# Kernel optimization log

Hardware: AMD Instinct MI355X
Metric: run time of the kernel (lower is better)

## Reference

```python
import jax, jax.numpy as jnp
import numpy as np

N_NODES = 50000


def gcn_conv(x, W, b, src, dst, norm, n):
    # PyG GCNConv: h = x W; out[dst] += norm * h[src]; out += b
    h = x @ W  # [N, out_dim]
    msg = h[src] * norm[:, None]  # [E+N, out_dim]
    out = jax.ops.segment_sum(msg, dst, num_segments=n)
    return out + b


def _norm_coeffs(src, dst, n):
    # symmetric normalization D^-1/2 A_hat D^-1/2 (self-loops already appended)
    deg = jax.ops.segment_sum(jnp.ones(src.shape[0], jnp.float32), dst, num_segments=n)
    dis = jnp.where(deg > 0, jax.lax.rsqrt(jnp.maximum(deg, 1.0)), 0.0)
    return dis[src] * dis[dst]


def setup_inputs() -> dict:
    key = jax.random.key(0)
    ks = jax.random.split(key, 8)
    n, e = N_NODES, 640000
    d_in, d_h, d_out = 128, 128, 64
    x = jax.random.normal(ks[0], (n, d_in), jnp.float32)
    edge_index = jax.random.randint(ks[1], (2, e), 0, n, jnp.int64)
    def glorot(k, shape):
        lim = np.sqrt(6.0 / (shape[0] + shape[1]))
        return jax.random.uniform(k, shape, jnp.float32, -lim, lim)
    return {
        "x": x,
        "edge_index": edge_index,
        "W1": glorot(ks[2], (d_in, d_h)), "b1": jnp.zeros((d_h,), jnp.float32),
        "W2": glorot(ks[3], (d_h, d_h)), "b2": jnp.zeros((d_h,), jnp.float32),
        "W3": glorot(ks[4], (d_h, d_out)), "b3": jnp.zeros((d_out,), jnp.float32),
    }


def reference(x, edge_index, W1, b1, W2, b2, W3, b3):
    n = x.shape[0]
    loop = jnp.arange(n, dtype=edge_index.dtype)
    src = jnp.concatenate([edge_index[0], loop])
    dst = jnp.concatenate([edge_index[1], loop])
    norm = _norm_coeffs(src, dst, n)
    h = jax.nn.relu(gcn_conv(x, W1, b1, src, dst, norm, n))
    h = jax.nn.relu(gcn_conv(h, W2, b2, src, dst, norm, n))
    return gcn_conv(h, W3, b3, src, dst, norm, n)
```

## Files before the change

kernel.cpp:

```cpp
#include <hip/hip_runtime.h>
#include <hip/hip_fp16.h>

typedef _Float16 f16x8 __attribute__((ext_vector_type(8)));
typedef float f32x4 __attribute__((ext_vector_type(4)));


__global__ void k_init(int* __restrict__ deg32, int nDeg,
                       unsigned int* __restrict__ ellw, int nEllw,
                       unsigned int pat) {
    int i = blockIdx.x * blockDim.x + threadIdx.x;
    if (i < nDeg) deg32[i] = 0;
    if (i < nEllw) ellw[i] = pat;
}

__global__ __launch_bounds__(256) void k_ellfill(const int* __restrict__ src,
                                                 const int* __restrict__ dst,
                                                 int* __restrict__ deg32,
                                                 unsigned short* __restrict__ ell, int E) {
    int e = blockIdx.x * blockDim.x + threadIdx.x;
    if (e >= E) return;
    int d = dst[e];
    int c = atomicAdd(&deg32[d << 4], 1);
    if (c < 64) ell[(size_t)d * 64 + c] = (unsigned short)src[e];
}

template <int BN, int NT, bool IN_F32>
__global__ __launch_bounds__(256) void k_gemm_mfma(const void* __restrict__ Xv,
                                                   const float* __restrict__ W,
                                                   const int* __restrict__ deg32,
                                                   _Float16* __restrict__ G, int N) {
    if (blockIdx.x == 0 && threadIdx.x < BN / 2)
        ((int*)(G + (size_t)N * BN))[threadIdx.x] = 0;

    const int lane = threadIdx.x & 63;
    const int wv = threadIdx.x >> 6;
    const int lo = lane & 15;
    const int kg = lane >> 4;
    const int colbase = wv * NT * 16;

    f16x8 b[4][NT];
#pragma unroll
    for (int t = 0; t < 4; ++t)
#pragma unroll
        for (int u = 0; u < NT; ++u)
#pragma unroll
            for (int j = 0; j < 8; ++j)
                b[t][u][j] = (_Float16)W[(size_t)(t * 32 + kg * 8 + j) * BN +
                                         colbase + u * 16 + lo];

    const float* Xf = (const float*)Xv;
    const _Float16* Xh = (const _Float16*)Xv;

    const int nslabs = N >> 4;
    for (int slab = blockIdx.x; slab < nslabs; slab += gridDim.x) {
        const int arow = slab * 16 + lo;
        f32x4 acc[NT];
#pragma unroll
        for (int u = 0; u < NT; ++u) acc[u] = (f32x4)0.0f;

#pragma unroll
        for (int t = 0; t < 4; ++t) {
            f16x8 a;
            if constexpr (IN_F32) {
                const float4* xp = (const float4*)&Xf[(size_t)arow * 128 + t * 32 + kg * 8];
                float4 u0 = xp[0], u1 = xp[1];
                a[0] = (_Float16)u0.x; a[1] = (_Float16)u0.y;
                a[2] = (_Float16)u0.z; a[3] = (_Float16)u0.w;
                a[4] = (_Float16)u1.x; a[5] = (_Float16)u1.y;
                a[6] = (_Float16)u1.z; a[7] = (_Float16)u1.w;
            } else {
                a = *(const f16x8*)&Xh[(size_t)arow * 128 + t * 32 + kg * 8];
            }
#pragma unroll
            for (int u = 0; u < NT; ++u)
                acc[u] = __builtin_amdgcn_mfma_f32_16x16x32_f16(a, b[t][u], acc[u], 0, 0, 0);
        }

        float ds[4];
#pragma unroll
        for (int r = 0; r < 4; ++r)
            ds[r] = rsqrtf((float)(deg32[(slab * 16 + kg * 4 + r) << 4] + 1));

#pragma unroll
        for (int u = 0; u < NT; ++u) {
            int col = colbase + u * 16 + lo;
#pragma unroll
            for (int r = 0; r < 4; ++r) {
                int row = slab * 16 + kg * 4 + r;
                G[(size_t)row * BN + col] = (_Float16)(acc[u][r] * ds[r]);
            }
        }
    }
}

__global__ __launch_bounds__(256) void k_aggr128(const int* __restrict__ deg32,
                                                 const unsigned short* __restrict__ ell,
                                                 const __half* __restrict__ gin,
                                                 const float* __restrict__ bias,
                                                 __half* __restrict__ out, int N) {
    int wid = blockIdx.x * 4 + (threadIdx.x >> 6);
    int lane = threadIdx.x & 63;
    if (wid >= N) return;
    int d = deg32[wid << 4];
    int dc = min(d, 64);
    int dp = (dc + 15) & ~15;

    const __half2* gp = (const __half2*)gin;
    float2 self = __half22float2(gp[(size_t)wid * 64 + lane]);

    const uint4* rowq = (const uint4*)&ell[(size_t)wid * 64];
    __half2 s0 = __float2half2_rn(0.f), s1 = s0, s2 = s0, s3 = s0;

    for (int j = 0; j < dp; j += 16) {
        uint4 r0 = rowq[j >> 3];
        uint4 r1 = rowq[(j >> 3) + 1];
        unsigned w[8] = {r0.x, r0.y, r0.z, r0.w, r1.x, r1.y, r1.z, r1.w};
        __half2 v[16];
#pragma unroll
        for (int t = 0; t < 16; ++t) {
            unsigned idx = (w[t >> 1] >> ((t & 1) * 16)) & 0xFFFFu;
            v[t] = gp[(size_t)idx * 64 + lane];
        }
#pragma unroll
        for (int t = 0; t < 16; t += 4) {
            s0 = __hadd2(s0, v[t + 0]);
            s1 = __hadd2(s1, v[t + 1]);
            s2 = __hadd2(s2, v[t + 2]);
            s3 = __hadd2(s3, v[t + 3]);
        }
    }

    float2 a0 = __half22float2(s0), a1 = __half22float2(s1);
    float2 a2 = __half22float2(s2), a3 = __half22float2(s3);
    float ax = self.x + (a0.x + a1.x) + (a2.x + a3.x);
    float ay = self.y + (a0.y + a1.y) + (a2.y + a3.y);

    float di = rsqrtf((float)(d + 1));
    float2 bv = *(const float2*)&bias[lane * 2];
    ax = fmaxf(di * ax + bv.x, 0.f);
    ay = fmaxf(di * ay + bv.y, 0.f);
    ((__half2*)out)[(size_t)wid * 64 + lane] = __float22half2_rn(make_float2(ax, ay));
}

__global__ __launch_bounds__(256) void k_aggr_final(const int* __restrict__ deg32,
                                                    const unsigned short* __restrict__ ell,
                                                    const __half* __restrict__ g,
                                                    const float* __restrict__ bias,
                                                    float* __restrict__ out, int N) {
    int wid = blockIdx.x * 8 + (threadIdx.x >> 5);
    int sub = threadIdx.x & 31;
    if (wid >= N) return;
    int d = deg32[wid << 4];
    int dc = min(d, 64);
    int dp = (dc + 15) & ~15;

    const __half2* gp = (const __half2*)g;
    float2 self = __half22float2(gp[(size_t)wid * 32 + sub]);

    const uint4* rowq = (const uint4*)&ell[(size_t)wid * 64];
    __half2 s0 = __float2half2_rn(0.f), s1 = s0, s2 = s0, s3 = s0;

    for (int j = 0; j < dp; j += 16) {
        uint4 r0 = rowq[j >> 3];
        uint4 r1 = rowq[(j >> 3) + 1];
        unsigned w[8] = {r0.x, r0.y, r0.z, r0.w, r1.x, r1.y, r1.z, r1.w};
        __half2 v[16];
#pragma unroll
        for (int t = 0; t < 16; ++t) {
            unsigned idx = (w[t >> 1] >> ((t & 1) * 16)) & 0xFFFFu;
            v[t] = gp[(size_t)idx * 32 + sub];
        }
#pragma unroll
        for (int t = 0; t < 16; t += 4) {
            s0 = __hadd2(s0, v[t + 0]);
            s1 = __hadd2(s1, v[t + 1]);
            s2 = __hadd2(s2, v[t + 2]);
            s3 = __hadd2(s3, v[t + 3]);
        }
    }

    float2 a0 = __half22float2(s0), a1 = __half22float2(s1);
    float2 a2 = __half22float2(s2), a3 = __half22float2(s3);
    float ax = self.x + (a0.x + a1.x) + (a2.x + a3.x);
    float ay = self.y + (a0.y + a1.y) + (a2.y + a3.y);

    float di = rsqrtf((float)(d + 1));
    float2 bv = *(const float2*)&bias[sub * 2];
    float2 o;
    o.x = di * ax + bv.x;
    o.y = di * ay + bv.y;
    *(float2*)&out[(size_t)wid * 64 + sub * 2] = o;
}

extern "C" void kernel_launch(void* const* d_in, const int* in_sizes, int n_in,
                              void* d_out, int out_size, void* d_ws, size_t ws_size,
                              hipStream_t stream) {
    const float* x = (const float*)d_in[0];
    const int* ei = (const int*)d_in[1];
    const float* W1 = (const float*)d_in[2];
    const float* b1 = (const float*)d_in[3];
    const float* W2 = (const float*)d_in[4];
    const float* b2 = (const float*)d_in[5];
    const float* W3 = (const float*)d_in[6];
    const float* b3 = (const float*)d_in[7];

    const int N = in_sizes[0] / 128;
    const int E = in_sizes[1] / 2;
    const int* src = ei;
    const int* dst = ei + E;

    auto align512 = [](size_t v) { return (v + 511) & ~(size_t)511; };
    char* p = (char*)d_ws;
    int* deg32 = (int*)p;                      p += align512((size_t)(N + 1) * 16 * 4);
    unsigned short* ell = (unsigned short*)p;  p += align512((size_t)N * 64 * 2);
    __half* bufA = (__half*)p;                 p += align512((size_t)(N + 1) * 128 * 2);
    __half* bufB = (__half*)p;

    const int ablocks = (N + 3) / 4;
    const int gemmBlocks = 512;

    int nDeg = (N + 1) * 16;
    int nEllw = N * 32;
    unsigned int pat = ((unsigned)N << 16) | (unsigned)N;
    int initThreads = nDeg > nEllw ? nDeg : nEllw;
    k_init<<<(initThreads + 255) / 256, 256, 0, stream>>>(deg32, nDeg,
                                                          (unsigned int*)ell, nEllw, pat);
    k_ellfill<<<(E + 255) / 256, 256, 0, stream>>>(src, dst, deg32, ell, E);
    k_gemm_mfma<128, 2, true><<<gemmBlocks, 256, 0, stream>>>(x, W1, deg32,
                                                              (_Float16*)bufA, N);
    k_aggr128<<<ablocks, 256, 0, stream>>>(deg32, ell, bufA, b1, bufB, N);
    k_gemm_mfma<128, 2, false><<<gemmBlocks, 256, 0, stream>>>(bufB, W2, deg32,
                                                               (_Float16*)bufA, N);
    k_aggr128<<<ablocks, 256, 0, stream>>>(deg32, ell, bufA, b2, bufB, N);
    k_gemm_mfma<64, 1, false><<<gemmBlocks, 256, 0, stream>>>(bufB, W3, deg32,
                                                              (_Float16*)bufA, N);
    k_aggr_final<<<(N + 7) / 8, 256, 0, stream>>>(deg32, ell, bufA, b3,
                                                  (float*)d_out, N);
}
```

Baseline: 144.4 us.

## Fuse layer aggregation with the next layer's GEMM via shared memory

The separate aggregation and GEMM kernels for layers 1-2 and 2-3 are merged into a single kernel. Each 1024-thread block aggregates 16 nodes (one wave per node) into LDS, then runs MFMA against the next weight matrix and writes the degree-scaled fp16 result. This removes a full round trip of the intermediate activation through global memory and two kernel launches. In exchange, every block reloads and converts the weight matrix and only some waves do GEMM work. The grid of N/16 also assumes N is a multiple of 16.

New measurement: 137.0 us. 1.05x faster.

```diff
diff --git a/kernel.cpp b/kernel.cpp
--- a/kernel.cpp
+++ b/kernel.cpp
@@ -24,55 +24,46 @@
     if (c < 64) ell[(size_t)d * 64 + c] = (unsigned short)src[e];
 }
 
-template <int BN, int NT, bool IN_F32>
-__global__ __launch_bounds__(256) void k_gemm_mfma(const void* __restrict__ Xv,
-                                                   const float* __restrict__ W,
-                                                   const int* __restrict__ deg32,
-                                                   _Float16* __restrict__ G, int N) {
-    if (blockIdx.x == 0 && threadIdx.x < BN / 2)
-        ((int*)(G + (size_t)N * BN))[threadIdx.x] = 0;
+__global__ __launch_bounds__(256) void k_gemm1(const float* __restrict__ X,
+                                               const float* __restrict__ W,
+                                               const int* __restrict__ deg32,
+                                               _Float16* __restrict__ G, int N) {
+    if (blockIdx.x == 0 && threadIdx.x < 64)
+        ((int*)(G + (size_t)N * 128))[threadIdx.x] = 0;
 
     const int lane = threadIdx.x & 63;
     const int wv = threadIdx.x >> 6;
     const int lo = lane & 15;
     const int kg = lane >> 4;
-    const int colbase = wv * NT * 16;
-
-    f16x8 b[4][NT];
+    const int colbase = wv * 32;
+
+    f16x8 b[4][2];
 #pragma unroll
     for (int t = 0; t < 4; ++t)
 #pragma unroll
-        for (int u = 0; u < NT; ++u)
+        for (int u = 0; u < 2; ++u)
 #pragma unroll
             for (int j = 0; j < 8; ++j)
-                b[t][u][j] = (_Float16)W[(size_t)(t * 32 + kg * 8 + j) * BN +
+                b[t][u][j] = (_Float16)W[(size_t)(t * 32 + kg * 8 + j) * 128 +
                                          colbase + u * 16 + lo];
-
-    const float* Xf = (const float*)Xv;
-    const _Float16* Xh = (const _Float16*)Xv;
 
     const int nslabs = N >> 4;
     for (int slab = blockIdx.x; slab < nslabs; slab += gridDim.x) {
         const int arow = slab * 16 + lo;
-        f32x4 acc[NT];
-#pragma unroll
-        for (int u = 0; u < NT; ++u) acc[u] = (f32x4)0.0f;
-
+        f32x4 acc[2];
+        acc[0] = (f32x4)0.0f;
+        acc[1] = (f32x4)0.0f;
 #pragma unroll
         for (int t = 0; t < 4; ++t) {
+            const float4* xp = (const float4*)&X[(size_t)arow * 128 + t * 32 + kg * 8];
+            float4 u0 = xp[0], u1 = xp[1];
             f16x8 a;
-            if constexpr (IN_F32) {
-                const float4* xp = (const float4*)&Xf[(size_t)arow * 128 + t * 32 + kg * 8];
-                float4 u0 = xp[0], u1 = xp[1];
-                a[0] = (_Float16)u0.x; a[1] = (_Float16)u0.y;
-                a[2] = (_Float16)u0.z; a[3] = (_Float16)u0.w;
-                a[4] = (_Float16)u1.x; a[5] = (_Float16)u1.y;
-                a[6] = (_Float16)u1.z; a[7] = (_Float16)u1.w;
-            } else {
-                a = *(const f16x8*)&Xh[(size_t)arow * 128 + t * 32 + kg * 8];
-            }
-#pragma unroll
-            for (int u = 0; u < NT; ++u)
+            a[0] = (_Float16)u0.x; a[1] = (_Float16)u0.y;
+            a[2] = (_Float16)u0.z; a[3] = (_Float16)u0.w;
+            a[4] = (_Float16)u1.x; a[5] = (_Float16)u1.y;
+            a[6] = (_Float16)u1.z; a[7] = (_Float16)u1.w;
+#pragma unroll
+            for (int u = 0; u < 2; ++u)
                 acc[u] = __builtin_amdgcn_mfma_f32_16x16x32_f16(a, b[t][u], acc[u], 0, 0, 0);
         }
 
@@ -82,64 +73,101 @@
             ds[r] = rsqrtf((float)(deg32[(slab * 16 + kg * 4 + r) << 4] + 1));
 
 #pragma unroll
-        for (int u = 0; u < NT; ++u) {
+        for (int u = 0; u < 2; ++u) {
             int col = colbase + u * 16 + lo;
 #pragma unroll
             for (int r = 0; r < 4; ++r) {
                 int row = slab * 16 + kg * 4 + r;
-                G[(size_t)row * BN + col] = (_Float16)(acc[u][r] * ds[r]);
+                G[(size_t)row * 128 + col] = (_Float16)(acc[u][r] * ds[r]);
             }
         }
     }
 }
 
-__global__ __launch_bounds__(256) void k_aggr128(const int* __restrict__ deg32,
-                                                 const unsigned short* __restrict__ ell,
-                                                 const __half* __restrict__ gin,
-                                                 const float* __restrict__ bias,
-                                                 __half* __restrict__ out, int N) {
-    int wid = blockIdx.x * 4 + (threadIdx.x >> 6);
-    int lane = threadIdx.x & 63;
-    if (wid >= N) return;
-    int d = deg32[wid << 4];
-    int dc = min(d, 64);
-    int dp = (dc + 15) & ~15;
-
-    const __half2* gp = (const __half2*)gin;
-    float2 self = __half22float2(gp[(size_t)wid * 64 + lane]);
-
-    const uint4* rowq = (const uint4*)&ell[(size_t)wid * 64];
-    __half2 s0 = __float2half2_rn(0.f), s1 = s0, s2 = s0, s3 = s0;
-
-    for (int j = 0; j < dp; j += 16) {
-        uint4 r0 = rowq[j >> 3];
-        uint4 r1 = rowq[(j >> 3) + 1];
-        unsigned w[8] = {r0.x, r0.y, r0.z, r0.w, r1.x, r1.y, r1.z, r1.w};
-        __half2 v[16];
-#pragma unroll
-        for (int t = 0; t < 16; ++t) {
-            unsigned idx = (w[t >> 1] >> ((t & 1) * 16)) & 0xFFFFu;
-            v[t] = gp[(size_t)idx * 64 + lane];
-        }
-#pragma unroll
-        for (int t = 0; t < 16; t += 4) {
-            s0 = __hadd2(s0, v[t + 0]);
-            s1 = __hadd2(s1, v[t + 1]);
-            s2 = __hadd2(s2, v[t + 2]);
-            s3 = __hadd2(s3, v[t + 3]);
-        }
-    }
-
-    float2 a0 = __half22float2(s0), a1 = __half22float2(s1);
-    float2 a2 = __half22float2(s2), a3 = __half22float2(s3);
-    float ax = self.x + (a0.x + a1.x) + (a2.x + a3.x);
-    float ay = self.y + (a0.y + a1.y) + (a2.y + a3.y);
-
-    float di = rsqrtf((float)(d + 1));
-    float2 bv = *(const float2*)&bias[lane * 2];
-    ax = fmaxf(di * ax + bv.x, 0.f);
-    ay = fmaxf(di * ay + bv.y, 0.f);
-    ((__half2*)out)[(size_t)wid * 64 + lane] = __float22half2_rn(make_float2(ax, ay));
+template <int BN>
+__global__ __launch_bounds__(1024, 8) void k_aggr_gemm(
+    const int* __restrict__ deg32, const unsigned short* __restrict__ ell,
+    const __half* __restrict__ gin, const float* __restrict__ bias,
+    const float* __restrict__ W, _Float16* __restrict__ gout, int N) {
+    __shared__ _Float16 As[16][136];
+
+    const int wv = threadIdx.x >> 6;
+    const int lane = threadIdx.x & 63;
+
+    if (blockIdx.x == 0 && threadIdx.x < BN / 2)
+        ((int*)(gout + (size_t)N * BN))[threadIdx.x] = 0;
+
+    const int base = blockIdx.x * 16;
+    const int wid = base + wv;
+    {
+        int d = deg32[wid << 4];
+        int dc = min(d, 64);
+        int dp = (dc + 15) & ~15;
+
+        const __half2* gp = (const __half2*)gin;
+        float2 self = __half22float2(gp[(size_t)wid * 64 + lane]);
+
+        const uint4* rowq = (const uint4*)&ell[(size_t)wid * 64];
+        __half2 s0 = __float2half2_rn(0.f), s1 = s0, s2 = s0, s3 = s0;
+
+        for (int j = 0; j < dp; j += 16) {
+            uint4 r0 = rowq[j >> 3];
+            uint4 r1 = rowq[(j >> 3) + 1];
+            unsigned w[8] = {r0.x, r0.y, r0.z, r0.w, r1.x, r1.y, r1.z, r1.w};
+            __half2 v[16];
+#pragma unroll
+            for (int t = 0; t < 16; ++t) {
+                unsigned idx = (w[t >> 1] >> ((t & 1) * 16)) & 0xFFFFu;
+                v[t] = gp[(size_t)idx * 64 + lane];
+            }
+#pragma unroll
+            for (int t = 0; t < 16; t += 4) {
+                s0 = __hadd2(s0, v[t + 0]);
+                s1 = __hadd2(s1, v[t + 1]);
+                s2 = __hadd2(s2, v[t + 2]);
+                s3 = __hadd2(s3, v[t + 3]);
+            }
+        }
+
+        float2 a0 = __half22float2(s0), a1 = __half22float2(s1);
+        float2 a2 = __half22float2(s2), a3 = __half22float2(s3);
+        float ax = self.x + (a0.x + a1.x) + (a2.x + a3.x);
+        float ay = self.y + (a0.y + a1.y) + (a2.y + a3.y);
+
+        float di = rsqrtf((float)(d + 1));
+        float2 bv = *(const float2*)&bias[lane * 2];
+        ax = fmaxf(di * ax + bv.x, 0.f);
+        ay = fmaxf(di * ay + bv.y, 0.f);
+        ((__half2*)&As[wv][0])[lane] = __float22half2_rn(make_float2(ax, ay));
+    }
+    __syncthreads();
+
+    if (wv < BN / 16) {
+        const int lo = lane & 15;
+        const int kg = lane >> 4;
+        const int col = wv * 16 + lo;
+
+        f16x8 b[4];
+#pragma unroll
+        for (int t = 0; t < 4; ++t)
+#pragma unroll
+            for (int j = 0; j < 8; ++j)
+                b[t][j] = (_Float16)W[(size_t)(t * 32 + kg * 8 + j) * BN + col];
+
+        f32x4 acc = (f32x4)0.0f;
+#pragma unroll
+        for (int t = 0; t < 4; ++t) {
+            f16x8 a = *(const f16x8*)&As[lo][t * 32 + kg * 8];
+            acc = __builtin_amdgcn_mfma_f32_16x16x32_f16(a, b[t], acc, 0, 0, 0);
+        }
+
+#pragma unroll
+        for (int r = 0; r < 4; ++r) {
+            int row = base + kg * 4 + r;
+            float ds = rsqrtf((float)(deg32[row << 4] + 1));
+            gout[(size_t)row * BN + col] = (_Float16)(acc[r] * ds);
+        }
+    }
 }
 
 __global__ __launch_bounds__(256) void k_aggr_final(const int* __restrict__ deg32,
@@ -216,9 +244,6 @@
     __half* bufA = (__half*)p;                 p += align512((size_t)(N + 1) * 128 * 2);
     __half* bufB = (__half*)p;
 
-    const int ablocks = (N + 3) / 4;
-    const int gemmBlocks = 512;
-
     int nDeg = (N + 1) * 16;
     int nEllw = N * 32;
     unsigned int pat = ((unsigned)N << 16) | (unsigned)N;
@@ -226,14 +251,11 @@
     k_init<<<(initThreads + 255) / 256, 256, 0, stream>>>(deg32, nDeg,
                                                           (unsigned int*)ell, nEllw, pat);
     k_ellfill<<<(E + 255) / 256, 256, 0, stream>>>(src, dst, deg32, ell, E);
-    k_gemm_mfma<128, 2, true><<<gemmBlocks, 256, 0, stream>>>(x, W1, deg32,
-                                                              (_Float16*)bufA, N);
-    k_aggr128<<<ablocks, 256, 0, stream>>>(deg32, ell, bufA, b1, bufB, N);
-    k_gemm_mfma<128, 2, false><<<gemmBlocks, 256, 0, stream>>>(bufB, W2, deg32,
-                                                               (_Float16*)bufA, N);
-    k_aggr128<<<ablocks, 256, 0, stream>>>(deg32, ell, bufA, b2, bufB, N);
-    k_gemm_mfma<64, 1, false><<<gemmBlocks, 256, 0, stream>>>(bufB, W3, deg32,
-                                                              (_Float16*)bufA, N);
+    k_gemm1<<<512, 256, 0, stream>>>(x, W1, deg32, (_Float16*)bufA, N);
+    k_aggr_gemm<128><<<N / 16, 1024, 0, stream>>>(deg32, ell, bufA, b1, W2,
+                                                  (_Float16*)bufB, N);
+    k_aggr_gemm<64><<<N / 16, 1024, 0, stream>>>(deg32, ell, bufB, b2, W3,
+                                                 (_Float16*)bufA, N);
     k_aggr_final<<<(N + 7) / 8, 256, 0, stream>>>(deg32, ell, bufA, b3,
                                                   (float*)d_out, N);
 }
```
